# Optimization experiments

Measured on AMD Instinct MI355X. Metric: run time of the kernel, lower is better.

## Reference

```python
import jax, jax.numpy as jnp
import numpy as np

N_HEAD = 12
NEG_INF = -1e30


def setup_inputs() -> dict:
    key = jax.random.key(0)
    ks = jax.random.split(key, 12)
    bs, q_len, c_len, d = 2, 2048, 2048, 768
    s = 1.0 / np.sqrt(d)
    return {
        "query": jax.random.normal(ks[0], (bs, q_len, d), jnp.float32),
        "context": jax.random.normal(ks[1], (bs, c_len, d), jnp.float32),
        "c_mask": jax.random.randint(ks[2], (bs, c_len), 0, 2, jnp.int32),
        "Wq_w": jax.random.normal(ks[3], (d, d), jnp.float32) * s,
        "Wq_b": jnp.zeros((d,), jnp.float32),
        "Wk_w": jax.random.normal(ks[4], (d, d), jnp.float32) * s,
        "Wk_b": jnp.zeros((d,), jnp.float32),
        "Wv_w": jax.random.normal(ks[5], (d, d), jnp.float32) * s,
        "Wv_b": jnp.zeros((d,), jnp.float32),
        "fc_w": jax.random.normal(ks[6], (d, d), jnp.float32) * s,
        "fc_b": jnp.zeros((d,), jnp.float32),
    }


def reference(query, context, c_mask, Wq_w, Wq_b, Wk_w, Wk_b, Wv_w, Wv_b, fc_w, fc_b):
    bs, q_len, d = query.shape
    c_len = context.shape[1]
    d_k = d // N_HEAD
    a = 1.0 / np.sqrt(d_k)

    # QKV projections (torch Linear: y = x @ W.T + b), split into heads
    q = (query @ Wq_w.T + Wq_b).reshape(bs, q_len, N_HEAD, d_k)
    k = (context @ Wk_w.T + Wk_b).reshape(bs, c_len, N_HEAD, d_k)
    v = (context @ Wv_w.T + Wv_b).reshape(bs, c_len, N_HEAD, d_k)

    # scores [bs, n_head, q_len, c_len]
    s = jnp.einsum('bqhd,bchd->bhqc', q, k) * a

    # mask_logits: s * m + (1 - m) * -1e30, mask broadcast over heads and q
    m = c_mask.astype(s.dtype)[:, None, None, :]
    s = s * m + (1.0 - m) * NEG_INF

    p = jax.nn.softmax(s, axis=-1)  # dropout p=0.0 -> identity

    out = jnp.einsum('bhqc,bchd->bqhd', p, v).reshape(bs, q_len, d)
    return out @ fc_w.T + fc_b
```

## Files before the change

kernel.cpp:

```cpp
#include <hip/hip_runtime.h>
#include <cstdint>

#define D_MODEL 768
#define NH      12
#define DKH     64
#define SEQ     2048
#define BS      2
#define MROWS   (BS*SEQ)

typedef __bf16 bf16x8 __attribute__((ext_vector_type(8)));
typedef float  f32x4  __attribute__((ext_vector_type(4)));
typedef unsigned int u32_as1 __attribute__((address_space(1)));
typedef unsigned int u32_as3 __attribute__((address_space(3)));

__device__ __forceinline__ void gld16(const void* g, void* l) {
  __builtin_amdgcn_global_load_lds((const u32_as1*)g, (u32_as3*)l, 16, 0, 0);
}
__device__ __forceinline__ unsigned short f2bf(float x) {
  return __builtin_bit_cast(unsigned short, (__bf16)x);
}

__global__ void cvt2(const float* __restrict__ a, const float* __restrict__ b,
                     unsigned short* __restrict__ oa, unsigned short* __restrict__ ob) {
  const float* in = blockIdx.y ? b : a;
  unsigned short* out = blockIdx.y ? ob : oa;
  int i = blockIdx.x * 256 + threadIdx.x;
  float4 v = reinterpret_cast<const float4*>(in)[i];
  ushort4 o; o.x = f2bf(v.x); o.y = f2bf(v.y); o.z = f2bf(v.z); o.w = f2bf(v.w);
  reinterpret_cast<ushort4*>(out)[i] = o;
}
__global__ void cvt4(const float* __restrict__ a, const float* __restrict__ b,
                     const float* __restrict__ c, const float* __restrict__ d,
                     unsigned short* __restrict__ oa, unsigned short* __restrict__ ob,
                     unsigned short* __restrict__ oc, unsigned short* __restrict__ od) {
  const float* in; unsigned short* out;
  switch (blockIdx.y) {
    case 0: in = a; out = oa; break;
    case 1: in = b; out = ob; break;
    case 2: in = c; out = oc; break;
    default: in = d; out = od; break;
  }
  int i = blockIdx.x * 256 + threadIdx.x;
  float4 v = reinterpret_cast<const float4*>(in)[i];
  ushort4 o; o.x = f2bf(v.x); o.y = f2bf(v.y); o.z = f2bf(v.z); o.w = f2bf(v.w);
  reinterpret_cast<ushort4*>(out)[i] = o;
}

template<bool OUT_F32, bool BIAS_ROW, bool FAST_IS_N>
__global__ __launch_bounds__(256, 4) void gemm_nt(
    const unsigned short* __restrict__ A, const unsigned short* __restrict__ B,
    const float* __restrict__ bias, void* __restrict__ Cout,
    int M, int N, int K)
{
  __shared__ alignas(16) char sA[2][8192];
  __shared__ alignas(16) char sB[2][8192];
  const int tid = threadIdx.x;
  const int w = tid >> 6, l = tid & 63;
  const int g16 = l >> 4, c16 = l & 15;
  const int flat = blockIdx.x;
  const int lin = (flat & 7) * 96 + (flat >> 3);
  const int tf = lin % 12, ts = lin / 12;
  const int m0 = (FAST_IS_N ? ts : tf) * 64;
  const int n0 = (FAST_IS_N ? tf : ts) * 64;
  const int wr = (w >> 1) * 32, wc = (w & 1) * 32;

  auto stage = [&](const unsigned short* __restrict__ P, int kt, char* dst) {
#pragma unroll
    for (int i = 0; i < 2; i++) {
      int ch = w * 2 + i;
      int X = ch * 1024 + l * 16;
      int row = X >> 7;
      int sl = ((X >> 4) & 7) ^ (row & 7);
      gld16(P + (size_t)row * K + kt + sl * 8, dst + ch * 1024);
    }
  };

  f32x4 acc[2][2];
#pragma unroll
  for (int m = 0; m < 2; m++)
#pragma unroll
    for (int n = 0; n < 2; n++) acc[m][n] = f32x4{0.f, 0.f, 0.f, 0.f};

  stage(A + (size_t)m0 * K, 0, sA[0]);
  stage(B + (size_t)n0 * K, 0, sB[0]);
  __syncthreads();
  int cur = 0;
  for (int kt = 0; kt < K; kt += 64) {
    if (kt + 64 < K) {
      stage(A + (size_t)m0 * K, kt + 64, sA[cur ^ 1]);
      stage(B + (size_t)n0 * K, kt + 64, sB[cur ^ 1]);
    }
    __builtin_amdgcn_s_setprio(1);
#pragma unroll
    for (int kk = 0; kk < 2; kk++) {
      bf16x8 af[2], bq[2];
#pragma unroll
      for (int m = 0; m < 2; m++) {
        int row = wr + m * 16 + c16, slot = kk * 4 + g16;
        af[m] = *(const bf16x8*)(sA[cur] + row * 128 + ((slot ^ (row & 7)) << 4));
      }
#pragma unroll
      for (int n = 0; n < 2; n++) {
        int row = wc + n * 16 + c16, slot = kk * 4 + g16;
        bq[n] = *(const bf16x8*)(sB[cur] + row * 128 + ((slot ^ (row & 7)) << 4));
      }
#pragma unroll
      for (int m = 0; m < 2; m++)
#pragma unroll
        for (int n = 0; n < 2; n++)
          acc[m][n] = __builtin_amdgcn_mfma_f32_16x16x32_bf16(af[m], bq[n], acc[m][n], 0, 0, 0);
    }
    __builtin_amdgcn_s_setprio(0);
    __syncthreads();
    cur ^= 1;
  }

#pragma unroll
  for (int m = 0; m < 2; m++)
#pragma unroll
    for (int n = 0; n < 2; n++)
#pragma unroll
      for (int r = 0; r < 4; r++) {
        int row = m0 + wr + m * 16 + g16 * 4 + r;
        int col = n0 + wc + n * 16 + c16;
        float v = acc[m][n][r] + (BIAS_ROW ? bias[row] : bias[col]);
        if constexpr (OUT_F32) ((float*)Cout)[(size_t)row * N + col] = v;
        else ((unsigned short*)Cout)[(size_t)row * N + col] = f2bf(v);
      }
}

__global__ __launch_bounds__(256, 4) void attn_kernel(
    const unsigned short* __restrict__ Qb, const unsigned short* __restrict__ Kb,
    const unsigned short* __restrict__ Vt, const int* __restrict__ cmask,
    unsigned short* __restrict__ Ob)
{
  __shared__ alignas(16) char sK[2][8192];
  __shared__ alignas(16) char sV[2][8192];
  __shared__ alignas(16) char sP[8192];
  const int tid = threadIdx.x, w = tid >> 6, l = tid & 63;
  const int g16 = l >> 4, c16 = l & 15;
  const int flat = blockIdx.x;
  const int xcd = flat & 7, sidx = flat >> 3;
  const int p = xcd + 8 * (sidx >> 5);
  const int qt = sidx & 31;
  const int h = p % 12, b = p / 12;
  const int qrow0 = b * SEQ + qt * 64;
  const int crow0 = b * SEQ;

  bf16x8 qa[2];
  {
    const unsigned short* qp =
        Qb + (size_t)(qrow0 + w * 16 + c16) * D_MODEL + h * DKH + g16 * 8;
    qa[0] = *(const bf16x8*)(qp);
    qa[1] = *(const bf16x8*)(qp + 32);
  }

  auto stageK = [&](int ct, int buf) {
#pragma unroll
    for (int i = 0; i < 2; i++) {
      int ch = w * 2 + i;
      int X = ch * 1024 + l * 16;
      int row = X >> 7;
      int sl = ((X >> 4) & 7) ^ (row & 7);
      gld16(Kb + (size_t)(crow0 + ct + row) * D_MODEL + h * DKH + sl * 8,
            sK[buf] + ch * 1024);
    }
  };
  auto stageV = [&](int ct, int buf) {
#pragma unroll
    for (int i = 0; i < 2; i++) {
      int ch = w * 2 + i;
      int X = ch * 1024 + l * 16;
      int row = X >> 7;
      int sl = ((X >> 4) & 7) ^ (row & 7);
      gld16(Vt + (size_t)(h * DKH + row) * (size_t)MROWS + crow0 + ct + sl * 8,
            sV[buf] + ch * 1024);
    }
  };

  f32x4 accO[4], accL;
#pragma unroll
  for (int n = 0; n < 4; n++) accO[n] = f32x4{0.f, 0.f, 0.f, 0.f};
  accL = f32x4{0.f, 0.f, 0.f, 0.f};
  const __bf16 one = (__bf16)1.0f;
  const bf16x8 vones = {one, one, one, one, one, one, one, one};

  stageK(0, 0); stageV(0, 0);
  __syncthreads();
  int cur = 0;

  for (int ct = 0; ct < SEQ; ct += 64) {
    if (ct + 64 < SEQ) { stageK(ct + 64, cur ^ 1); stageV(ct + 64, cur ^ 1); }

    int mk[4];
#pragma unroll
    for (int n = 0; n < 4; n++) mk[n] = cmask[crow0 + ct + n * 16 + c16];

    f32x4 s[4];
#pragma unroll
    for (int n = 0; n < 4; n++) s[n] = f32x4{0.f, 0.f, 0.f, 0.f};
    __builtin_amdgcn_s_setprio(1);
#pragma unroll
    for (int kk = 0; kk < 2; kk++) {
      bf16x8 kf[4];
#pragma unroll
      for (int n = 0; n < 4; n++) {
        int row = n * 16 + c16, slot = kk * 4 + g16;
        kf[n] = *(const bf16x8*)(sK[cur] + row * 128 + ((slot ^ (row & 7)) << 4));
      }
#pragma unroll
      for (int n = 0; n < 4; n++)
        s[n] = __builtin_amdgcn_mfma_f32_16x16x32_bf16(qa[kk], kf[n], s[n], 0, 0, 0);
    }
    __builtin_amdgcn_s_setprio(0);

#pragma unroll
    for (int r = 0; r < 4; r++) {
      int prow = g16 * 4 + r;
#pragma unroll
      for (int n = 0; n < 4; n++) {
        float pv = mk[n] ? __expf(s[n][r] * 0.125f) : 0.f;
        int slot = n * 2 + (c16 >> 3);
        int addr = w * 2048 + prow * 128 + ((slot ^ (prow & 7)) << 4) + (c16 & 7) * 2;
        *(__bf16*)(sP + addr) = (__bf16)pv;
      }
    }

    __builtin_amdgcn_s_setprio(1);
#pragma unroll
    for (int kk = 0; kk < 2; kk++) {
      bf16x8 pa, vf[4];
      {
        int prow = c16, slot = kk * 4 + g16;
        pa = *(const bf16x8*)(sP + w * 2048 + prow * 128 + ((slot ^ (prow & 7)) << 4));
      }
#pragma unroll
      for (int n = 0; n < 4; n++) {
        int vrow = n * 16 + c16, slot = kk * 4 + g16;
        vf[n] = *(const bf16x8*)(sV[cur] + vrow * 128 + ((slot ^ (vrow & 7)) << 4));
      }
#pragma unroll
      for (int n = 0; n < 4; n++)
        accO[n] = __builtin_amdgcn_mfma_f32_16x16x32_bf16(pa, vf[n], accO[n], 0, 0, 0);
      accL = __builtin_amdgcn_mfma_f32_16x16x32_bf16(pa, vones, accL, 0, 0, 0);
    }
    __builtin_amdgcn_s_setprio(0);

    __syncthreads();
    cur ^= 1;
  }

#pragma unroll
  for (int r = 0; r < 4; r++) {
    float inv = 1.0f / accL[r];
#pragma unroll
    for (int n = 0; n < 4; n++) {
      int row = qrow0 + w * 16 + g16 * 4 + r;
      int col = h * DKH + n * 16 + c16;
      Ob[(size_t)row * D_MODEL + col] = f2bf(accO[n][r] * inv);
    }
  }
}

extern "C" void kernel_launch(void* const* d_in, const int* in_sizes, int n_in,
                              void* d_out, int out_size, void* d_ws, size_t ws_size,
                              hipStream_t stream) {
  const float* query   = (const float*)d_in[0];
  const float* context = (const float*)d_in[1];
  const int*   cmask   = (const int*)d_in[2];
  const float* Wq_w = (const float*)d_in[3];
  const float* Wq_b = (const float*)d_in[4];
  const float* Wk_w = (const float*)d_in[5];
  const float* Wk_b = (const float*)d_in[6];
  const float* Wv_w = (const float*)d_in[7];
  const float* Wv_b = (const float*)d_in[8];
  const float* fc_w = (const float*)d_in[9];
  const float* fc_b = (const float*)d_in[10];
  float* out = (float*)d_out;

  unsigned short* ws   = (unsigned short*)d_ws;
  const size_t NQ = (size_t)MROWS * D_MODEL;
  const size_t NW = (size_t)D_MODEL * D_MODEL;
  unsigned short* q_bf = ws;
  unsigned short* c_bf = q_bf + NQ;
  unsigned short* Qb   = c_bf + NQ;
  unsigned short* Kb   = Qb + NQ;
  unsigned short* Vtb  = Kb + NQ;
  unsigned short* Ob   = Vtb + NQ;
  unsigned short* wq   = Ob + NQ;
  unsigned short* wk   = wq + NW;
  unsigned short* wv   = wk + NW;
  unsigned short* wf   = wv + NW;

  cvt2<<<dim3(NQ / 4 / 256, 2), 256, 0, stream>>>(query, context, q_bf, c_bf);
  cvt4<<<dim3(NW / 4 / 256, 4), 256, 0, stream>>>(Wq_w, Wk_w, Wv_w, fc_w, wq, wk, wv, wf);

  gemm_nt<false, false, true><<<768, 256, 0, stream>>>(
      q_bf, wq, Wq_b, Qb, MROWS, D_MODEL, D_MODEL);
  gemm_nt<false, false, true><<<768, 256, 0, stream>>>(
      c_bf, wk, Wk_b, Kb, MROWS, D_MODEL, D_MODEL);
  gemm_nt<false, true, false><<<768, 256, 0, stream>>>(
      wv, c_bf, Wv_b, Vtb, D_MODEL, MROWS, D_MODEL);

  attn_kernel<<<768, 256, 0, stream>>>(Qb, Kb, Vtb, cmask, Ob);

  gemm_nt<true, false, true><<<768, 256, 0, stream>>>(
      Ob, wf, fc_b, out, MROWS, D_MODEL, D_MODEL);
}
```

Baseline: 107.6 us.

## Use 128x128 GEMM tiles and merge Q/K/V projections into one launch

```diff
diff --git a/kernel.cpp b/kernel.cpp
--- a/kernel.cpp
+++ b/kernel.cpp
@@ -46,68 +46,63 @@
   reinterpret_cast<ushort4*>(out)[i] = o;
 }
 
-template<bool OUT_F32, bool BIAS_ROW, bool FAST_IS_N>
-__global__ __launch_bounds__(256, 4) void gemm_nt(
+template<bool OUT_F32>
+__device__ __forceinline__ void gemm128_body(
     const unsigned short* __restrict__ A, const unsigned short* __restrict__ B,
-    const float* __restrict__ bias, void* __restrict__ Cout,
-    int M, int N, int K)
+    const float* __restrict__ bias, int biasRow, void* __restrict__ Cout,
+    int ldc, int m0, int n0)
 {
-  __shared__ alignas(16) char sA[2][8192];
-  __shared__ alignas(16) char sB[2][8192];
+  __shared__ alignas(16) char sA[2][16384];
+  __shared__ alignas(16) char sB[2][16384];
   const int tid = threadIdx.x;
   const int w = tid >> 6, l = tid & 63;
   const int g16 = l >> 4, c16 = l & 15;
-  const int flat = blockIdx.x;
-  const int lin = (flat & 7) * 96 + (flat >> 3);
-  const int tf = lin % 12, ts = lin / 12;
-  const int m0 = (FAST_IS_N ? ts : tf) * 64;
-  const int n0 = (FAST_IS_N ? tf : ts) * 64;
-  const int wr = (w >> 1) * 32, wc = (w & 1) * 32;
-
-  auto stage = [&](const unsigned short* __restrict__ P, int kt, char* dst) {
-#pragma unroll
-    for (int i = 0; i < 2; i++) {
-      int ch = w * 2 + i;
+  const int wr = (w >> 1) * 64, wc = (w & 1) * 64;
+
+  auto stage = [&](const unsigned short* __restrict__ P, int p0, int kt, char* dst) {
+#pragma unroll
+    for (int i = 0; i < 4; i++) {
+      int ch = w * 4 + i;
       int X = ch * 1024 + l * 16;
       int row = X >> 7;
       int sl = ((X >> 4) & 7) ^ (row & 7);
-      gld16(P + (size_t)row * K + kt + sl * 8, dst + ch * 1024);
+      gld16(P + (size_t)(p0 + row) * 768 + kt + sl * 8, dst + ch * 1024);
     }
   };
 
-  f32x4 acc[2][2];
-#pragma unroll
-  for (int m = 0; m < 2; m++)
-#pragma unroll
-    for (int n = 0; n < 2; n++) acc[m][n] = f32x4{0.f, 0.f, 0.f, 0.f};
-
-  stage(A + (size_t)m0 * K, 0, sA[0]);
-  stage(B + (size_t)n0 * K, 0, sB[0]);
+  f32x4 acc[4][4];
+#pragma unroll
+  for (int m = 0; m < 4; m++)
+#pragma unroll
+    for (int n = 0; n < 4; n++) acc[m][n] = f32x4{0.f, 0.f, 0.f, 0.f};
+
+  stage(A, m0, 0, sA[0]);
+  stage(B, n0, 0, sB[0]);
   __syncthreads();
   int cur = 0;
-  for (int kt = 0; kt < K; kt += 64) {
-    if (kt + 64 < K) {
-      stage(A + (size_t)m0 * K, kt + 64, sA[cur ^ 1]);
-      stage(B + (size_t)n0 * K, kt + 64, sB[cur ^ 1]);
+  for (int kt = 0; kt < 768; kt += 64) {
+    if (kt + 64 < 768) {
+      stage(A, m0, kt + 64, sA[cur ^ 1]);
+      stage(B, n0, kt + 64, sB[cur ^ 1]);
     }
     __builtin_amdgcn_s_setprio(1);
 #pragma unroll
     for (int kk = 0; kk < 2; kk++) {
-      bf16x8 af[2], bq[2];
-#pragma unroll
-      for (int m = 0; m < 2; m++) {
+      bf16x8 af[4], bq[4];
+#pragma unroll
+      for (int m = 0; m < 4; m++) {
         int row = wr + m * 16 + c16, slot = kk * 4 + g16;
         af[m] = *(const bf16x8*)(sA[cur] + row * 128 + ((slot ^ (row & 7)) << 4));
       }
 #pragma unroll
-      for (int n = 0; n < 2; n++) {
+      for (int n = 0; n < 4; n++) {
         int row = wc + n * 16 + c16, slot = kk * 4 + g16;
         bq[n] = *(const bf16x8*)(sB[cur] + row * 128 + ((slot ^ (row & 7)) << 4));
       }
 #pragma unroll
-      for (int m = 0; m < 2; m++)
-#pragma unroll
-        for (int n = 0; n < 2; n++)
+      for (int m = 0; m < 4; m++)
+#pragma unroll
+        for (int n = 0; n < 4; n++)
           acc[m][n] = __builtin_amdgcn_mfma_f32_16x16x32_bf16(af[m], bq[n], acc[m][n], 0, 0, 0);
     }
     __builtin_amdgcn_s_setprio(0);
@@ -116,17 +111,49 @@
   }
 
 #pragma unroll
-  for (int m = 0; m < 2; m++)
-#pragma unroll
-    for (int n = 0; n < 2; n++)
+  for (int m = 0; m < 4; m++)
+#pragma unroll
+    for (int n = 0; n < 4; n++)
 #pragma unroll
       for (int r = 0; r < 4; r++) {
         int row = m0 + wr + m * 16 + g16 * 4 + r;
         int col = n0 + wc + n * 16 + c16;
-        float v = acc[m][n][r] + (BIAS_ROW ? bias[row] : bias[col]);
-        if constexpr (OUT_F32) ((float*)Cout)[(size_t)row * N + col] = v;
-        else ((unsigned short*)Cout)[(size_t)row * N + col] = f2bf(v);
-      }
+        float v = acc[m][n][r] + (biasRow ? bias[row] : bias[col]);
+        if constexpr (OUT_F32) ((float*)Cout)[(size_t)row * ldc + col] = v;
+        else ((unsigned short*)Cout)[(size_t)row * ldc + col] = f2bf(v);
+      }
+}
+
+__global__ __launch_bounds__(256, 2) void gemm_qkv(
+    const unsigned short* __restrict__ q_bf, const unsigned short* __restrict__ c_bf,
+    const unsigned short* __restrict__ wq, const unsigned short* __restrict__ wk,
+    const unsigned short* __restrict__ wv,
+    const float* __restrict__ bq, const float* __restrict__ bk,
+    const float* __restrict__ bv,
+    unsigned short* __restrict__ Qb, unsigned short* __restrict__ Kb,
+    unsigned short* __restrict__ Vtb)
+{
+  const int x = blockIdx.x;
+  const int lin = (x & 7) * 24 + (x >> 3);
+  const int tf = lin % 6, ts = lin / 6;
+  const unsigned short *A, *B; const float* bias; unsigned short* C;
+  int m0, n0, ldc, biasRow;
+  switch (blockIdx.y) {
+    case 0:  A = q_bf; B = wq;   bias = bq; C = Qb;  m0 = ts*128; n0 = tf*128; ldc = 768;  biasRow = 0; break;
+    case 1:  A = c_bf; B = wk;   bias = bk; C = Kb;  m0 = ts*128; n0 = tf*128; ldc = 768;  biasRow = 0; break;
+    default: A = wv;   B = c_bf; bias = bv; C = Vtb; m0 = tf*128; n0 = ts*128; ldc = 4096; biasRow = 1; break;
+  }
+  gemm128_body<false>(A, B, bias, biasRow, C, ldc, m0, n0);
+}
+
+__global__ __launch_bounds__(256, 2) void gemm_fc(
+    const unsigned short* __restrict__ Ob, const unsigned short* __restrict__ wf,
+    const float* __restrict__ fb, float* __restrict__ out)
+{
+  const int x = blockIdx.x;
+  const int lin = (x & 7) * 24 + (x >> 3);
+  const int tf = lin % 6, ts = lin / 6;
+  gemm128_body<true>(Ob, wf, fb, 0, out, 768, ts * 128, tf * 128);
 }
 
 __global__ __launch_bounds__(256, 4) void attn_kernel(
@@ -295,15 +322,10 @@
   cvt2<<<dim3(NQ / 4 / 256, 2), 256, 0, stream>>>(query, context, q_bf, c_bf);
   cvt4<<<dim3(NW / 4 / 256, 4), 256, 0, stream>>>(Wq_w, Wk_w, Wv_w, fc_w, wq, wk, wv, wf);
 
-  gemm_nt<false, false, true><<<768, 256, 0, stream>>>(
-      q_bf, wq, Wq_b, Qb, MROWS, D_MODEL, D_MODEL);
-  gemm_nt<false, false, true><<<768, 256, 0, stream>>>(
-      c_bf, wk, Wk_b, Kb, MROWS, D_MODEL, D_MODEL);
-  gemm_nt<false, true, false><<<768, 256, 0, stream>>>(
-      wv, c_bf, Wv_b, Vtb, D_MODEL, MROWS, D_MODEL);
+  gemm_qkv<<<dim3(192, 3), 256, 0, stream>>>(
+      q_bf, c_bf, wq, wk, wv, Wq_b, Wk_b, Wv_b, Qb, Kb, Vtb);
 
   attn_kernel<<<768, 256, 0, stream>>>(Qb, Kb, Vtb, cmask, Ob);
 
-  gemm_nt<true, false, true><<<768, 256, 0, stream>>>(
-      Ob, wf, fc_b, out, MROWS, D_MODEL, D_MODEL);
-}
+  gemm_fc<<<192, 256, 0, stream>>>(Ob, wf, fc_b, out);
+}
```

Result: no change. 105.7 us (-1.7%).
